# Kernel tuning notes

Measured on AMD Instinct MI355X. Metric: run time of the kernel, lower is better.

## Reference

```python
import jax, jax.numpy as jnp
import numpy as np

T, B, D_IN, H, ALPHA = 512, 32, 41, 800, 20
BOND_LENS = np.array([1.458, 1.525, 1.330], dtype=np.float32)   # N-CA, CA-C, C-N (Angstrom)
BOND_ANGS = np.array([2.124, 1.941, 2.028], dtype=np.float32)   # supplementary bond angles (rad)


def _lstm_dir(x, Wih, Whh, b, reverse):
    # x: [T,B,in] -> hidden states [T,B,H] for one direction
    xs = jnp.einsum('tbi,gi->tbg', x, Wih) + b  # precompute input projections [T,B,4H]
    if reverse:
        xs = xs[::-1]
    h0 = jnp.zeros((x.shape[1], Whh.shape[1]), x.dtype)

    def step(carry, xg):
        h, c = carry
        g = xg + h @ Whh.T
        i, f, gg, o = jnp.split(g, 4, axis=-1)
        c = jax.nn.sigmoid(f) * c + jax.nn.sigmoid(i) * jnp.tanh(gg)
        h = jax.nn.sigmoid(o) * jnp.tanh(c)
        return (h, c), h

    _, hs = jax.lax.scan(step, (h0, h0), xs)
    return hs[::-1] if reverse else hs


def _bilstm(x, Wf, Uf, bf, Wb, Ub, bb):
    return jnp.concatenate([_lstm_dir(x, Wf, Uf, bf, False),
                            _lstm_dir(x, Wb, Ub, bb, True)], axis=-1)


def _calculate_dihedrals(p, alphabet):
    # p: [T,B,ALPHA] softmax weights; alphabet: [ALPHA,3] learned angles
    y = p @ jnp.sin(alphabet)
    xc = p @ jnp.cos(alphabet)
    return jnp.arctan2(y, xc)  # [T,B,3]


def _calculate_coordinates(angles):
    # NeRF-style recursive extension: 3 backbone atoms per residue.
    t, b, _ = angles.shape
    tors = angles.transpose(0, 2, 1).reshape(3 * t, b)          # [3T,B]
    r = jnp.tile(jnp.asarray(BOND_LENS), t)                      # [3T]
    th = jnp.tile(jnp.asarray(BOND_ANGS), t)                     # [3T]
    a0 = jnp.broadcast_to(jnp.array([0.0, 0.0, 0.0], angles.dtype), (b, 3))
    b0 = jnp.broadcast_to(jnp.array([1.458, 0.0, 0.0], angles.dtype), (b, 3))
    c0 = jnp.broadcast_to(jnp.array([2.0, 1.0, 0.0], angles.dtype), (b, 3))

    def _norm(v):
        return v / jnp.linalg.norm(v, axis=-1, keepdims=True)

    def step(carry, inp):
        pa, pb, pc = carry
        phi, rr, tt = inp                                        # phi:[B], rr/tt scalar
        bc = _norm(pc - pb)
        n = _norm(jnp.cross(pb - pa, bc))
        m = jnp.cross(n, bc)
        d = (pc - rr * jnp.cos(tt) * bc
             + (rr * jnp.sin(tt)) * (jnp.cos(phi)[:, None] * m + jnp.sin(phi)[:, None] * n))
        return (pb, pc, d), d

    _, coords = jax.lax.scan(step, (a0, b0, c0), (tors, r, th))
    return coords  # [3T,B,3]


def setup_inputs() -> dict:
    key = jax.random.key(0)
    ks = jax.random.split(key, 16)
    s = 0.05
    d = {"x": jax.random.normal(ks[0], (T, B, D_IN), jnp.float32)}
    ins = [D_IN, 2 * H]
    i = 1
    for l in range(2):
        for dname in ("f", "b"):
            d[f"Wih_{dname}{l}"] = jax.random.normal(ks[i], (4 * H, ins[l]), jnp.float32) * s; i += 1
            d[f"Whh_{dname}{l}"] = jax.random.normal(ks[i], (4 * H, H), jnp.float32) * s; i += 1
            d[f"b_{dname}{l}"] = jnp.zeros((4 * H,), jnp.float32)
    d["Wl"] = jax.random.normal(ks[13], (ALPHA, 2 * H), jnp.float32) * s
    d["bl"] = jnp.zeros((ALPHA,), jnp.float32)
    d["alphabet"] = jax.random.uniform(ks[14], (ALPHA, 3), jnp.float32, -np.pi, np.pi)
    return d


def reference(x, Wih_f0, Whh_f0, b_f0, Wih_b0, Whh_b0, b_b0,
              Wih_f1, Whh_f1, b_f1, Wih_b1, Whh_b1, b_b1,
              Wl, bl, alphabet):
    h1 = _bilstm(x, Wih_f0, Whh_f0, b_f0, Wih_b0, Whh_b0, b_b0)   # [T,B,2H]
    h2 = _bilstm(h1, Wih_f1, Whh_f1, b_f1, Wih_b1, Whh_b1, b_b1)  # [T,B,2H]
    logits = jnp.einsum('tbh,ah->tba', h2, Wl) + bl
    p = jax.nn.softmax(logits, axis=-1)
    angles = _calculate_dihedrals(p, alphabet)                     # [T,B,3]
    return _calculate_coordinates(angles)                          # [3T,B,3]
```

## Files before the change

### kernel.cpp

```cpp
#include <hip/hip_runtime.h>
#include <math.h>


#define TT 512
#define BB 32
#define HH 800
#define DIN 41
#define KROW 1600

typedef _Float16 f16;
typedef _Float16 half8 __attribute__((ext_vector_type(8)));
typedef float floatx4 __attribute__((ext_vector_type(4)));
typedef unsigned uint4v __attribute__((ext_vector_type(4)));

#define OFF_XT   8192
#define OFF_H1   (OFF_XT + 524288)
#define OFF_H2   (OFF_H1 + 13107200)
#define OFF_ANG  (OFF_H2 + 13107200)
#define OFF_SIN  (OFF_ANG + 49152)
#define OFF_COS  (OFF_SIN + 64)

#define SENT 0xFFFFFFFFFFFFFFFFull

__device__ __forceinline__ float sigm(float x) { return 1.0f / (1.0f + expf(-x)); }

union U64H8 { unsigned long long u[2]; half8 h; };

__device__ __forceinline__ unsigned long long ald8(const f16* p) {
    return __hip_atomic_load((const unsigned long long*)p, __ATOMIC_RELAXED, __HIP_MEMORY_SCOPE_AGENT);
}
__device__ __forceinline__ void ast8(f16* p, unsigned long long v) {
    __hip_atomic_store((unsigned long long*)p, v, __ATOMIC_RELAXED, __HIP_MEMORY_SCOPE_AGENT);
}
__device__ __forceinline__ half8 cvt8(const float* p) {
    half8 r;
#pragma unroll
    for (int i = 0; i < 8; ++i) r[i] = (f16)p[i];
    return r;
}

__device__ __forceinline__ size_t hpi(int t, int KT, int q, int b) {
    return ((((size_t)t * 50 + KT) * 4 + q) * 32 + b) * 8;
}

__global__ __launch_bounds__(512, 1) void rnn0_kernel(
    const f16* __restrict__ xp, f16* __restrict__ h1,
    const float* __restrict__ Wih_f0, const float* __restrict__ Whh_f0, const float* __restrict__ b_f0,
    const float* __restrict__ Wih_b0, const float* __restrict__ Whh_b0, const float* __restrict__ b_b0)
{
    __shared__ float gbuf[8][32][34];
    __shared__ f16  hbuf[256];

    const int tid  = threadIdx.x;
    const int w    = tid >> 6;
    const int lane = tid & 63;
    const int l15  = lane & 15;
    const int quad = lane >> 4;
    const int dir  = blockIdx.x / 100;
    const int blk  = blockIdx.x % 100;
    const int j0   = blk * 8;
    const int jl   = tid >> 5;
    const int bb   = tid & 31;

    const float* Wih = dir ? Wih_b0 : Wih_f0;
    const float* Whh = dir ? Whh_b0 : Whh_f0;
    const float* bs  = dir ? b_b0  : b_f0;

    half8 afr[2][4];
#pragma unroll
    for (int mt = 0; mt < 2; ++mt) {
        const int r = mt * 16 + l15;
        const int grow = (r >> 3) * HH + j0 + (r & 7);
#pragma unroll
        for (int i = 0; i < 4; ++i) {
            const int kt = w + 8 * i;
            half8 v;
#pragma unroll
            for (int jj = 0; jj < 8; ++jj) v[jj] = (f16)0.f;
            if (kt < 27) {
                if (kt < 2) {
#pragma unroll
                    for (int jj = 0; jj < 8; ++jj) {
                        const int k = kt * 32 + quad * 8 + jj;
                        if (k < DIN) v[jj] = (f16)Wih[(size_t)grow * DIN + k];
                    }
                } else {
                    v = cvt8(Whh + (size_t)grow * HH + (kt - 2) * 32 + quad * 8);
                }
            }
            afr[mt][i] = v;
        }
    }
    const float bi = bs[0 * HH + j0 + jl], bf = bs[1 * HH + j0 + jl],
                bg = bs[2 * HH + j0 + jl], bo = bs[3 * HH + j0 + jl];

    const int KT0 = dir * 25 + (blk >> 2);
    const int q0  = blk & 3;

    half8 px0, px1;
    {
        const int t0 = dir ? (TT - 1) : 0;
        if (w < 2) {
            const f16* p = xp + ((((size_t)t0 * 2 + w) * 4 + quad) * 32) * 8;
            px0 = *(const half8*)(p + (size_t)l15 * 8);
            px1 = *(const half8*)(p + (size_t)(16 + l15) * 8);
        }
    }

    float creg = 0.0f;
    for (int s = 0; s < TT; ++s) {
        const int t  = dir ? (TT - 1 - s) : s;
        const int tp = dir ? t + 1 : t - 1;
        const int tn = dir ? (t > 0 ? t - 1 : 0) : (t < TT - 1 ? t + 1 : t);

        U64H8 rb[4][2];
        if (s > 0) {
#pragma unroll
            for (int i = 0; i < 4; ++i) {
                const int kt = w + 8 * i;
                if (kt >= 2 && kt < 27) {
                    const f16* p = h1 + hpi(tp, dir * 25 + (kt - 2), quad, 0);
                    rb[i][0].u[0] = ald8(p + (size_t)l15 * 8);
                    rb[i][0].u[1] = ald8(p + (size_t)l15 * 8 + 4);
                    rb[i][1].u[0] = ald8(p + (size_t)(16 + l15) * 8);
                    rb[i][1].u[1] = ald8(p + (size_t)(16 + l15) * 8 + 4);
                }
            }
        }

        floatx4 acc[2][2];
        acc[0][0] = (floatx4)0.f; acc[0][1] = (floatx4)0.f;
        acc[1][0] = (floatx4)0.f; acc[1][1] = (floatx4)0.f;

        if (w < 2) {
            acc[0][0] = __builtin_amdgcn_mfma_f32_16x16x32_f16(afr[0][0], px0, acc[0][0], 0, 0, 0);
            acc[0][1] = __builtin_amdgcn_mfma_f32_16x16x32_f16(afr[0][0], px1, acc[0][1], 0, 0, 0);
            acc[1][0] = __builtin_amdgcn_mfma_f32_16x16x32_f16(afr[1][0], px0, acc[1][0], 0, 0, 0);
            acc[1][1] = __builtin_amdgcn_mfma_f32_16x16x32_f16(afr[1][0], px1, acc[1][1], 0, 0, 0);
            const f16* p = xp + ((((size_t)tn * 2 + w) * 4 + quad) * 32) * 8;
            px0 = *(const half8*)(p + (size_t)l15 * 8);
            px1 = *(const half8*)(p + (size_t)(16 + l15) * 8);
        }

        if (s > 0) {
            int dm = 0;
#pragma unroll
            for (int i = 0; i < 4; ++i) {
                const int kt = w + 8 * i;
                if (kt >= 2 && kt < 27) {
                    const int bad = (rb[i][0].u[0] == SENT) | (rb[i][0].u[1] == SENT) |
                                    (rb[i][1].u[0] == SENT) | (rb[i][1].u[1] == SENT);
                    dm |= bad << i;
                }
            }
            while (__any(dm != 0)) {
#pragma unroll
                for (int i = 0; i < 4; ++i) {
                    const int kt = w + 8 * i;
                    if (kt >= 2 && kt < 27) {
                        if (dm & (1 << i)) {
                            const f16* p = h1 + hpi(tp, dir * 25 + (kt - 2), quad, 0);
                            rb[i][0].u[0] = ald8(p + (size_t)l15 * 8);
                            rb[i][0].u[1] = ald8(p + (size_t)l15 * 8 + 4);
                            rb[i][1].u[0] = ald8(p + (size_t)(16 + l15) * 8);
                            rb[i][1].u[1] = ald8(p + (size_t)(16 + l15) * 8 + 4);
                        }
                    }
                }
                int nm = 0;
#pragma unroll
                for (int i = 0; i < 4; ++i) {
                    const int kt = w + 8 * i;
                    if (kt >= 2 && kt < 27) {
                        if (dm & (1 << i)) {
                            const int bad = (rb[i][0].u[0] == SENT) | (rb[i][0].u[1] == SENT) |
                                            (rb[i][1].u[0] == SENT) | (rb[i][1].u[1] == SENT);
                            nm |= bad << i;
                        }
                    }
                }
                dm = nm;
            }
#pragma unroll
            for (int i = 0; i < 4; ++i) {
                const int kt = w + 8 * i;
                if (kt >= 2 && kt < 27) {
                    acc[0][0] = __builtin_amdgcn_mfma_f32_16x16x32_f16(afr[0][i], rb[i][0].h, acc[0][0], 0, 0, 0);
                    acc[0][1] = __builtin_amdgcn_mfma_f32_16x16x32_f16(afr[0][i], rb[i][1].h, acc[0][1], 0, 0, 0);
                    acc[1][0] = __builtin_amdgcn_mfma_f32_16x16x32_f16(afr[1][i], rb[i][0].h, acc[1][0], 0, 0, 0);
                    acc[1][1] = __builtin_amdgcn_mfma_f32_16x16x32_f16(afr[1][i], rb[i][1].h, acc[1][1], 0, 0, 0);
                }
            }
        }

#pragma unroll
        for (int mt = 0; mt < 2; ++mt)
#pragma unroll
            for (int nt = 0; nt < 2; ++nt)
#pragma unroll
                for (int rg = 0; rg < 4; ++rg)
                    gbuf[w][mt * 16 + quad * 4 + rg][nt * 16 + l15] = acc[mt][nt][rg];
        __syncthreads();
        if (tid < 256) {
            float gi_ = bi, gf_ = bf, gc_ = bg, go_ = bo;
#pragma unroll
            for (int ww = 0; ww < 8; ++ww) {
                gi_ += gbuf[ww][jl][bb];
                gf_ += gbuf[ww][8 + jl][bb];
                gc_ += gbuf[ww][16 + jl][bb];
                go_ += gbuf[ww][24 + jl][bb];
            }
            const float cn = sigm(gf_) * creg + sigm(gi_) * tanhf(gc_);
            creg = cn;
            hbuf[bb * 8 + jl] = (f16)(sigm(go_) * tanhf(cn));
        }
        __syncthreads();
        if (tid < BB) {
            f16* dst = h1 + hpi(t, KT0, q0, tid);
            const unsigned long long* src = (const unsigned long long*)(hbuf + tid * 8);
            ast8(dst, src[0]);
            ast8(dst + 4, src[1]);
        }
    }
}

__global__ __launch_bounds__(512, 1) void rnn1_kernel(
    const f16* __restrict__ h1, f16* __restrict__ h2,
    const float* __restrict__ Wih_f1, const float* __restrict__ Whh_f1, const float* __restrict__ b_f1,
    const float* __restrict__ Wih_b1, const float* __restrict__ Whh_b1, const float* __restrict__ b_b1)
{
    __shared__ float gbuf[8][32][34];
    __shared__ f16  hbuf[256];

    const int tid  = threadIdx.x;
    const int w    = tid >> 6;
    const int lane = tid & 63;
    const int l15  = lane & 15;
    const int quad = lane >> 4;
    const int dir  = blockIdx.x / 100;
    const int blk  = blockIdx.x % 100;
    const int j0   = blk * 8;
    const int jl   = tid >> 5;
    const int bb   = tid & 31;

    const float* Wih = dir ? Wih_b1 : Wih_f1;
    const float* Whh = dir ? Whh_b1 : Whh_f1;
    const float* bs  = dir ? b_b1  : b_f1;

    half8 afr[2][10];
#pragma unroll
    for (int mt = 0; mt < 2; ++mt) {
        const int r = mt * 16 + l15;
        const int grow = (r >> 3) * HH + j0 + (r & 7);
#pragma unroll
        for (int i = 0; i < 10; ++i) {
            const int kt = w + 8 * i;
            half8 v;
#pragma unroll
            for (int jj = 0; jj < 8; ++jj) v[jj] = (f16)0.f;
            if (kt < 75) {
                if (kt < 50) v = cvt8(Wih + (size_t)grow * KROW + kt * 32 + quad * 8);
                else         v = cvt8(Whh + (size_t)grow * HH + (kt - 50) * 32 + quad * 8);
            }
            afr[mt][i] = v;
        }
    }
    const float bi = bs[0 * HH + j0 + jl], bf = bs[1 * HH + j0 + jl],
                bg = bs[2 * HH + j0 + jl], bo = bs[3 * HH + j0 + jl];

    const int KT0 = dir * 25 + (blk >> 2);
    const int q0  = blk & 3;

    half8 pa[7][2];
    {
        const int t0 = dir ? (TT - 1) : 0;
#pragma unroll
        for (int i = 0; i < 7; ++i) {
            const int kt = w + 8 * i;
            if (kt < 50) {
                const f16* p = h1 + hpi(t0, kt, quad, 0);
                pa[i][0] = *(const half8*)(p + (size_t)l15 * 8);
                pa[i][1] = *(const half8*)(p + (size_t)(16 + l15) * 8);
            }
        }
    }

    float creg = 0.0f;
    for (int s = 0; s < TT; ++s) {
        const int t  = dir ? (TT - 1 - s) : s;
        const int tp = dir ? t + 1 : t - 1;
        const int tn = dir ? (t > 0 ? t - 1 : 0) : (t < TT - 1 ? t + 1 : t);

        U64H8 rb[4][2];
        if (s > 0) {
#pragma unroll
            for (int i = 6; i < 10; ++i) {
                const int kt = w + 8 * i;
                if (kt >= 50 && kt < 75) {
                    const f16* p = h2 + hpi(tp, dir * 25 + (kt - 50), quad, 0);
                    rb[i - 6][0].u[0] = ald8(p + (size_t)l15 * 8);
                    rb[i - 6][0].u[1] = ald8(p + (size_t)l15 * 8 + 4);
                    rb[i - 6][1].u[0] = ald8(p + (size_t)(16 + l15) * 8);
                    rb[i - 6][1].u[1] = ald8(p + (size_t)(16 + l15) * 8 + 4);
                }
            }
        }

        floatx4 acc[2][2];
        acc[0][0] = (floatx4)0.f; acc[0][1] = (floatx4)0.f;
        acc[1][0] = (floatx4)0.f; acc[1][1] = (floatx4)0.f;

#pragma unroll
        for (int i = 0; i < 7; ++i) {
            const int kt = w + 8 * i;
            if (kt < 50) {
                acc[0][0] = __builtin_amdgcn_mfma_f32_16x16x32_f16(afr[0][i], pa[i][0], acc[0][0], 0, 0, 0);
                acc[0][1] = __builtin_amdgcn_mfma_f32_16x16x32_f16(afr[0][i], pa[i][1], acc[0][1], 0, 0, 0);
                acc[1][0] = __builtin_amdgcn_mfma_f32_16x16x32_f16(afr[1][i], pa[i][0], acc[1][0], 0, 0, 0);
                acc[1][1] = __builtin_amdgcn_mfma_f32_16x16x32_f16(afr[1][i], pa[i][1], acc[1][1], 0, 0, 0);
            }
        }

#pragma unroll
        for (int i = 0; i < 7; ++i) {
            const int kt = w + 8 * i;
            if (kt < 50) {
                const f16* p = h1 + hpi(tn, kt, quad, 0);
                pa[i][0] = *(const half8*)(p + (size_t)l15 * 8);
                pa[i][1] = *(const half8*)(p + (size_t)(16 + l15) * 8);
            }
        }

        if (s > 0) {
            int dm = 0;
#pragma unroll
            for (int i = 6; i < 10; ++i) {
                const int kt = w + 8 * i;
                if (kt >= 50 && kt < 75) {
                    const int bad = (rb[i - 6][0].u[0] == SENT) | (rb[i - 6][0].u[1] == SENT) |
                                    (rb[i - 6][1].u[0] == SENT) | (rb[i - 6][1].u[1] == SENT);
                    dm |= bad << (i - 6);
                }
            }
            while (__any(dm != 0)) {
#pragma unroll
                for (int i = 6; i < 10; ++i) {
                    const int kt = w + 8 * i;
                    if (kt >= 50 && kt < 75) {
                        if (dm & (1 << (i - 6))) {
                            const f16* p = h2 + hpi(tp, dir * 25 + (kt - 50), quad, 0);
                            rb[i - 6][0].u[0] = ald8(p + (size_t)l15 * 8);
                            rb[i - 6][0].u[1] = ald8(p + (size_t)l15 * 8 + 4);
                            rb[i - 6][1].u[0] = ald8(p + (size_t)(16 + l15) * 8);
                            rb[i - 6][1].u[1] = ald8(p + (size_t)(16 + l15) * 8 + 4);
                        }
                    }
                }
                int nm = 0;
#pragma unroll
                for (int i = 6; i < 10; ++i) {
                    const int kt = w + 8 * i;
                    if (kt >= 50 && kt < 75) {
                        if (dm & (1 << (i - 6))) {
                            const int bad = (rb[i - 6][0].u[0] == SENT) | (rb[i - 6][0].u[1] == SENT) |
                                            (rb[i - 6][1].u[0] == SENT) | (rb[i - 6][1].u[1] == SENT);
                            nm |= bad << (i - 6);
                        }
                    }
                }
                dm = nm;
            }
#pragma unroll
            for (int i = 6; i < 10; ++i) {
                const int kt = w + 8 * i;
                if (kt >= 50 && kt < 75) {
                    acc[0][0] = __builtin_amdgcn_mfma_f32_16x16x32_f16(afr[0][i], rb[i - 6][0].h, acc[0][0], 0, 0, 0);
                    acc[0][1] = __builtin_amdgcn_mfma_f32_16x16x32_f16(afr[0][i], rb[i - 6][1].h, acc[0][1], 0, 0, 0);
                    acc[1][0] = __builtin_amdgcn_mfma_f32_16x16x32_f16(afr[1][i], rb[i - 6][0].h, acc[1][0], 0, 0, 0);
                    acc[1][1] = __builtin_amdgcn_mfma_f32_16x16x32_f16(afr[1][i], rb[i - 6][1].h, acc[1][1], 0, 0, 0);
                }
            }
        }

#pragma unroll
        for (int mt = 0; mt < 2; ++mt)
#pragma unroll
            for (int nt = 0; nt < 2; ++nt)
#pragma unroll
                for (int rg = 0; rg < 4; ++rg)
                    gbuf[w][mt * 16 + quad * 4 + rg][nt * 16 + l15] = acc[mt][nt][rg];
        __syncthreads();
        if (tid < 256) {
            float gi_ = bi, gf_ = bf, gc_ = bg, go_ = bo;
#pragma unroll
            for (int ww = 0; ww < 8; ++ww) {
                gi_ += gbuf[ww][jl][bb];
                gf_ += gbuf[ww][8 + jl][bb];
                gc_ += gbuf[ww][16 + jl][bb];
                go_ += gbuf[ww][24 + jl][bb];
            }
            const float cn = sigm(gf_) * creg + sigm(gi_) * tanhf(gc_);
            creg = cn;
            hbuf[bb * 8 + jl] = (f16)(sigm(go_) * tanhf(cn));
        }
        __syncthreads();
        if (tid < BB) {
            f16* dst = h2 + hpi(t, KT0, q0, tid);
            const unsigned long long* src = (const unsigned long long*)(hbuf + tid * 8);
            ast8(dst, src[0]);
            ast8(dst + 4, src[1]);
        }
    }
}

__global__ void prep_kernel(const float* __restrict__ x, const float* __restrict__ alphabet,
                            f16* __restrict__ xp, float* __restrict__ sin_t,
                            float* __restrict__ cos_t, unsigned* __restrict__ hsent) {
    const int gid = blockIdx.x * blockDim.x + threadIdx.x;
    const int nth = gridDim.x * blockDim.x;
    for (int idx = gid; idx < TT * BB * 64; idx += nth) {
        const int tb = idx >> 6;
        const int i  = idx & 63;
        const int t  = tb >> 5;
        const int b  = tb & 31;
        const size_t di = ((((size_t)t * 2 + (i >> 5)) * 4 + ((i >> 3) & 3)) * 32 + b) * 8 + (i & 7);
        xp[di] = (i < DIN) ? (f16)x[(size_t)tb * DIN + i] : (f16)0.f;
    }
    uint4v* hs4 = (uint4v*)hsent;
    const uint4v sv = {0xFFFFFFFFu, 0xFFFFFFFFu, 0xFFFFFFFFu, 0xFFFFFFFFu};
    const int n4 = (2 * 13107200) / 4;
    for (int idx = gid; idx < n4; idx += nth) hs4[idx] = sv;
    if (gid < 60) { sin_t[gid] = sinf(alphabet[gid]); cos_t[gid] = cosf(alphabet[gid]); }
}

__global__ __launch_bounds__(640, 1) void head_kernel(
    const f16* __restrict__ h2, const float* __restrict__ Wl, const float* __restrict__ bl,
    const float* __restrict__ sin_t, const float* __restrict__ cos_t,
    float* __restrict__ angles) {
    __shared__ float pl[20][33];
    __shared__ float mx[32];
    const int t = blockIdx.x;
    const int a = threadIdx.x / 32;
    const int b = threadIdx.x & 31;
    if (a < 20) {
        float acc = bl[a];
        const float* wr = Wl + (size_t)a * KROW;
        const f16*   hr = h2 + (size_t)t * 50 * 4 * 32 * 8;
        for (int k8 = 0; k8 < KROW / 8; ++k8) {
            const half8 hv = *(const half8*)(hr + (((size_t)k8) * 32 + b) * 8);
#pragma unroll
            for (int j = 0; j < 8; ++j) acc = fmaf(wr[k8 * 8 + j], (float)hv[j], acc);
        }
        pl[a][b] = acc;
    }
    __syncthreads();
    if (threadIdx.x < 32) {
        float m = pl[0][threadIdx.x];
        for (int i = 1; i < 20; ++i) m = fmaxf(m, pl[i][threadIdx.x]);
        mx[threadIdx.x] = m;
    }
    __syncthreads();
    if (a < 20) pl[a][b] = expf(pl[a][b] - mx[b]);
    __syncthreads();
    if (threadIdx.x < 96) {
        const int c = threadIdx.x / 32, b2 = threadIdx.x & 31;
        float y = 0.f, xx = 0.f;
        for (int i = 0; i < 20; ++i) {
            const float e = pl[i][b2];
            y  = fmaf(e, sin_t[i * 3 + c], y);
            xx = fmaf(e, cos_t[i * 3 + c], xx);
        }
        angles[((size_t)t * BB + b2) * 3 + c] = atan2f(y, xx);
    }
}

__global__ void coords_kernel(const float* __restrict__ angles, float* __restrict__ out) {
    const int b = threadIdx.x;
    if (b >= BB) return;
    const float rs[3]  = {1.458f, 1.525f, 1.33f};
    const float ths[3] = {2.124f, 1.941f, 2.028f};
    float ct[3], st[3];
#pragma unroll
    for (int k = 0; k < 3; ++k) { ct[k] = cosf(ths[k]); st[k] = sinf(ths[k]); }
    float pax = 0.f,     pay = 0.f, paz = 0.f;
    float pbx = 1.458f,  pby = 0.f, pbz = 0.f;
    float pcx = 2.f,     pcy = 1.f, pcz = 0.f;
    for (int n = 0; n < 3 * TT; ++n) {
        const int t = n / 3;
        const int k = n - 3 * t;
        const float phi = angles[((size_t)t * BB + b) * 3 + k];
        float ux = pcx - pbx, uy = pcy - pby, uz = pcz - pbz;
        const float il = rsqrtf(ux * ux + uy * uy + uz * uz);
        const float bcx = ux * il, bcy = uy * il, bcz = uz * il;
        const float wx = pbx - pax, wy = pby - pay, wz = pbz - paz;
        float cx = wy * bcz - wz * bcy, cy = wz * bcx - wx * bcz, cz = wx * bcy - wy * bcx;
        const float iln = rsqrtf(cx * cx + cy * cy + cz * cz);
        const float nx = cx * iln, ny = cy * iln, nz = cz * iln;
        const float mxv = ny * bcz - nz * bcy, myv = nz * bcx - nx * bcz, mzv = nx * bcy - ny * bcx;
        float sp, cp;
        __sincosf(phi, &sp, &cp);
        const float rr = rs[k], cth = ct[k], sth = st[k];
        const float dx = pcx - rr * cth * bcx + rr * sth * (cp * mxv + sp * nx);
        const float dy = pcy - rr * cth * bcy + rr * sth * (cp * myv + sp * ny);
        const float dz = pcz - rr * cth * bcz + rr * sth * (cp * mzv + sp * nz);
        float* o = out + ((size_t)n * BB + b) * 3;
        o[0] = dx; o[1] = dy; o[2] = dz;
        pax = pbx; pay = pby; paz = pbz;
        pbx = pcx; pby = pcy; pbz = pcz;
        pcx = dx;  pcy = dy;  pcz = dz;
    }
}

extern "C" void kernel_launch(void* const* d_in, const int* in_sizes, int n_in,
                              void* d_out, int out_size, void* d_ws, size_t ws_size,
                              hipStream_t stream) {
    (void)in_sizes; (void)n_in; (void)out_size; (void)ws_size;
    const float* x      = (const float*)d_in[0];
    const float* Wih_f0 = (const float*)d_in[1];
    const float* Whh_f0 = (const float*)d_in[2];
    const float* b_f0   = (const float*)d_in[3];
    const float* Wih_b0 = (const float*)d_in[4];
    const float* Whh_b0 = (const float*)d_in[5];
    const float* b_b0   = (const float*)d_in[6];
    const float* Wih_f1 = (const float*)d_in[7];
    const float* Whh_f1 = (const float*)d_in[8];
    const float* b_f1   = (const float*)d_in[9];
    const float* Wih_b1 = (const float*)d_in[10];
    const float* Whh_b1 = (const float*)d_in[11];
    const float* b_b1   = (const float*)d_in[12];
    const float* Wl     = (const float*)d_in[13];
    const float* bl     = (const float*)d_in[14];
    const float* alphabet = (const float*)d_in[15];

    float* ws = (float*)d_ws;
    f16*   xp     = (f16*)(ws + OFF_XT);
    f16*   h1     = (f16*)(ws + OFF_H1);
    f16*   h2     = (f16*)(ws + OFF_H2);
    float* angles = ws + OFF_ANG;
    float* sin_t  = ws + OFF_SIN;
    float* cos_t  = ws + OFF_COS;

    prep_kernel<<<1024, 256, 0, stream>>>(x, alphabet, xp, sin_t, cos_t, (unsigned*)(ws + OFF_H1));
    rnn0_kernel<<<200, 512, 0, stream>>>(xp, h1,
        Wih_f0, Whh_f0, b_f0, Wih_b0, Whh_b0, b_b0);
    rnn1_kernel<<<200, 512, 0, stream>>>(h1, h2,
        Wih_f1, Whh_f1, b_f1, Wih_b1, Whh_b1, b_b1);
    head_kernel<<<TT, 640, 0, stream>>>(h2, Wl, bl, sin_t, cos_t, angles);
    coords_kernel<<<1, 64, 0, stream>>>(angles, (float*)d_out);
}
```

Measured before the change: 4.455 ms.

## Halve LSTM persistent blocks by assigning 16 hidden units per block

New measurement: 7.600 ms. 70.6% more time.

```diff
diff --git a/kernel.cpp b/kernel.cpp
--- a/kernel.cpp
+++ b/kernel.cpp
@@ -48,17 +48,17 @@
     const float* __restrict__ Wih_f0, const float* __restrict__ Whh_f0, const float* __restrict__ b_f0,
     const float* __restrict__ Wih_b0, const float* __restrict__ Whh_b0, const float* __restrict__ b_b0)
 {
-    __shared__ float gbuf[8][32][34];
-    __shared__ f16  hbuf[256];
+    __shared__ float gbuf[8][64][34];
+    __shared__ f16  hbuf[512];
 
     const int tid  = threadIdx.x;
     const int w    = tid >> 6;
     const int lane = tid & 63;
     const int l15  = lane & 15;
     const int quad = lane >> 4;
-    const int dir  = blockIdx.x / 100;
-    const int blk  = blockIdx.x % 100;
-    const int j0   = blk * 8;
+    const int dir  = blockIdx.x / 50;
+    const int blk  = blockIdx.x % 50;
+    const int j0   = blk * 16;
     const int jl   = tid >> 5;
     const int bb   = tid & 31;
 
@@ -66,11 +66,10 @@
     const float* Whh = dir ? Whh_b0 : Whh_f0;
     const float* bs  = dir ? b_b0  : b_f0;
 
-    half8 afr[2][4];
-#pragma unroll
-    for (int mt = 0; mt < 2; ++mt) {
-        const int r = mt * 16 + l15;
-        const int grow = (r >> 3) * HH + j0 + (r & 7);
+    half8 afr[4][4];
+#pragma unroll
+    for (int mt = 0; mt < 4; ++mt) {
+        const int grow = mt * HH + j0 + l15;
 #pragma unroll
         for (int i = 0; i < 4; ++i) {
             const int kt = w + 8 * i;
@@ -94,8 +93,9 @@
     const float bi = bs[0 * HH + j0 + jl], bf = bs[1 * HH + j0 + jl],
                 bg = bs[2 * HH + j0 + jl], bo = bs[3 * HH + j0 + jl];
 
-    const int KT0 = dir * 25 + (blk >> 2);
-    const int q0  = blk & 3;
+    const int g8   = blk * 2 + (tid >> 5);
+    const int sKT  = dir * 25 + (g8 >> 2);
+    const int sq   = g8 & 3;
 
     half8 px0, px1;
     {
@@ -128,15 +128,16 @@
             }
         }
 
-        floatx4 acc[2][2];
-        acc[0][0] = (floatx4)0.f; acc[0][1] = (floatx4)0.f;
-        acc[1][0] = (floatx4)0.f; acc[1][1] = (floatx4)0.f;
+        floatx4 acc[4][2];
+#pragma unroll
+        for (int mt = 0; mt < 4; ++mt) { acc[mt][0] = (floatx4)0.f; acc[mt][1] = (floatx4)0.f; }
 
         if (w < 2) {
-            acc[0][0] = __builtin_amdgcn_mfma_f32_16x16x32_f16(afr[0][0], px0, acc[0][0], 0, 0, 0);
-            acc[0][1] = __builtin_amdgcn_mfma_f32_16x16x32_f16(afr[0][0], px1, acc[0][1], 0, 0, 0);
-            acc[1][0] = __builtin_amdgcn_mfma_f32_16x16x32_f16(afr[1][0], px0, acc[1][0], 0, 0, 0);
-            acc[1][1] = __builtin_amdgcn_mfma_f32_16x16x32_f16(afr[1][0], px1, acc[1][1], 0, 0, 0);
+#pragma unroll
+            for (int mt = 0; mt < 4; ++mt) {
+                acc[mt][0] = __builtin_amdgcn_mfma_f32_16x16x32_f16(afr[mt][0], px0, acc[mt][0], 0, 0, 0);
+                acc[mt][1] = __builtin_amdgcn_mfma_f32_16x16x32_f16(afr[mt][0], px1, acc[mt][1], 0, 0, 0);
+            }
             const f16* p = xp + ((((size_t)tn * 2 + w) * 4 + quad) * 32) * 8;
             px0 = *(const half8*)(p + (size_t)l15 * 8);
             px1 = *(const half8*)(p + (size_t)(16 + l15) * 8);
@@ -185,39 +186,41 @@
             for (int i = 0; i < 4; ++i) {
                 const int kt = w + 8 * i;
                 if (kt >= 2 && kt < 27) {
-                    acc[0][0] = __builtin_amdgcn_mfma_f32_16x16x32_f16(afr[0][i], rb[i][0].h, acc[0][0], 0, 0, 0);
-                    acc[0][1] = __builtin_amdgcn_mfma_f32_16x16x32_f16(afr[0][i], rb[i][1].h, acc[0][1], 0, 0, 0);
-                    acc[1][0] = __builtin_amdgcn_mfma_f32_16x16x32_f16(afr[1][i], rb[i][0].h, acc[1][0], 0, 0, 0);
-                    acc[1][1] = __builtin_amdgcn_mfma_f32_16x16x32_f16(afr[1][i], rb[i][1].h, acc[1][1], 0, 0, 0);
-                }
-            }
-        }
-
-#pragma unroll
-        for (int mt = 0; mt < 2; ++mt)
+#pragma unroll
+                    for (int mt = 0; mt < 4; ++mt) {
+                        acc[mt][0] = __builtin_amdgcn_mfma_f32_16x16x32_f16(afr[mt][i], rb[i][0].h, acc[mt][0], 0, 0, 0);
+                        acc[mt][1] = __builtin_amdgcn_mfma_f32_16x16x32_f16(afr[mt][i], rb[i][1].h, acc[mt][1], 0, 0, 0);
+                    }
+                }
+            }
+        }
+
+#pragma unroll
+        for (int mt = 0; mt < 4; ++mt)
 #pragma unroll
             for (int nt = 0; nt < 2; ++nt)
 #pragma unroll
                 for (int rg = 0; rg < 4; ++rg)
                     gbuf[w][mt * 16 + quad * 4 + rg][nt * 16 + l15] = acc[mt][nt][rg];
         __syncthreads();
-        if (tid < 256) {
+        {
             float gi_ = bi, gf_ = bf, gc_ = bg, go_ = bo;
 #pragma unroll
             for (int ww = 0; ww < 8; ++ww) {
                 gi_ += gbuf[ww][jl][bb];
-                gf_ += gbuf[ww][8 + jl][bb];
-                gc_ += gbuf[ww][16 + jl][bb];
-                go_ += gbuf[ww][24 + jl][bb];
+                gf_ += gbuf[ww][16 + jl][bb];
+                gc_ += gbuf[ww][32 + jl][bb];
+                go_ += gbuf[ww][48 + jl][bb];
             }
             const float cn = sigm(gf_) * creg + sigm(gi_) * tanhf(gc_);
             creg = cn;
-            hbuf[bb * 8 + jl] = (f16)(sigm(go_) * tanhf(cn));
+            hbuf[bb * 16 + jl] = (f16)(sigm(go_) * tanhf(cn));
         }
         __syncthreads();
-        if (tid < BB) {
-            f16* dst = h1 + hpi(t, KT0, q0, tid);
-            const unsigned long long* src = (const unsigned long long*)(hbuf + tid * 8);
+        if (tid < 64) {
+            const int b = tid & 31;
+            f16* dst = h1 + hpi(t, sKT, sq, b);
+            const unsigned long long* src = (const unsigned long long*)(hbuf + b * 16 + (tid >> 5) * 8);
             ast8(dst, src[0]);
             ast8(dst + 4, src[1]);
         }
@@ -229,17 +232,17 @@
     const float* __restrict__ Wih_f1, const float* __restrict__ Whh_f1, const float* __restrict__ b_f1,
     const float* __restrict__ Wih_b1, const float* __restrict__ Whh_b1, const float* __restrict__ b_b1)
 {
-    __shared__ float gbuf[8][32][34];
-    __shared__ f16  hbuf[256];
+    __shared__ float gbuf[8][64][34];
+    __shared__ f16  hbuf[512];
 
     const int tid  = threadIdx.x;
     const int w    = tid >> 6;
     const int lane = tid & 63;
     const int l15  = lane & 15;
     const int quad = lane >> 4;
-    const int dir  = blockIdx.x / 100;
-    const int blk  = blockIdx.x % 100;
-    const int j0   = blk * 8;
+    const int dir  = blockIdx.x / 50;
+    const int blk  = blockIdx.x % 50;
+    const int j0   = blk * 16;
     const int jl   = tid >> 5;
     const int bb   = tid & 31;
 
@@ -247,11 +250,10 @@
     const float* Whh = dir ? Whh_b1 : Whh_f1;
     const float* bs  = dir ? b_b1  : b_f1;
 
-    half8 afr[2][10];
-#pragma unroll
-    for (int mt = 0; mt < 2; ++mt) {
-        const int r = mt * 16 + l15;
-        const int grow = (r >> 3) * HH + j0 + (r & 7);
+    half8 afr[4][10];
+#pragma unroll
+    for (int mt = 0; mt < 4; ++mt) {
+        const int grow = mt * HH + j0 + l15;
 #pragma unroll
         for (int i = 0; i < 10; ++i) {
             const int kt = w + 8 * i;
@@ -268,8 +270,9 @@
     const float bi = bs[0 * HH + j0 + jl], bf = bs[1 * HH + j0 + jl],
                 bg = bs[2 * HH + j0 + jl], bo = bs[3 * HH + j0 + jl];
 
-    const int KT0 = dir * 25 + (blk >> 2);
-    const int q0  = blk & 3;
+    const int g8   = blk * 2 + (tid >> 5);
+    const int sKT  = dir * 25 + (g8 >> 2);
+    const int sq   = g8 & 3;
 
     half8 pa[7][2];
     {
@@ -306,18 +309,19 @@
             }
         }
 
-        floatx4 acc[2][2];
-        acc[0][0] = (floatx4)0.f; acc[0][1] = (floatx4)0.f;
-        acc[1][0] = (floatx4)0.f; acc[1][1] = (floatx4)0.f;
+        floatx4 acc[4][2];
+#pragma unroll
+        for (int mt = 0; mt < 4; ++mt) { acc[mt][0] = (floatx4)0.f; acc[mt][1] = (floatx4)0.f; }
 
 #pragma unroll
         for (int i = 0; i < 7; ++i) {
             const int kt = w + 8 * i;
             if (kt < 50) {
-                acc[0][0] = __builtin_amdgcn_mfma_f32_16x16x32_f16(afr[0][i], pa[i][0], acc[0][0], 0, 0, 0);
-                acc[0][1] = __builtin_amdgcn_mfma_f32_16x16x32_f16(afr[0][i], pa[i][1], acc[0][1], 0, 0, 0);
-                acc[1][0] = __builtin_amdgcn_mfma_f32_16x16x32_f16(afr[1][i], pa[i][0], acc[1][0], 0, 0, 0);
-                acc[1][1] = __builtin_amdgcn_mfma_f32_16x16x32_f16(afr[1][i], pa[i][1], acc[1][1], 0, 0, 0);
+#pragma unroll
+                for (int mt = 0; mt < 4; ++mt) {
+                    acc[mt][0] = __builtin_amdgcn_mfma_f32_16x16x32_f16(afr[mt][i], pa[i][0], acc[mt][0], 0, 0, 0);
+                    acc[mt][1] = __builtin_amdgcn_mfma_f32_16x16x32_f16(afr[mt][i], pa[i][1], acc[mt][1], 0, 0, 0);
+                }
             }
         }
 
@@ -374,39 +378,41 @@
             for (int i = 6; i < 10; ++i) {
                 const int kt = w + 8 * i;
                 if (kt >= 50 && kt < 75) {
-                    acc[0][0] = __builtin_amdgcn_mfma_f32_16x16x32_f16(afr[0][i], rb[i - 6][0].h, acc[0][0], 0, 0, 0);
-                    acc[0][1] = __builtin_amdgcn_mfma_f32_16x16x32_f16(afr[0][i], rb[i - 6][1].h, acc[0][1], 0, 0, 0);
-                    acc[1][0] = __builtin_amdgcn_mfma_f32_16x16x32_f16(afr[1][i], rb[i - 6][0].h, acc[1][0], 0, 0, 0);
-                    acc[1][1] = __builtin_amdgcn_mfma_f32_16x16x32_f16(afr[1][i], rb[i - 6][1].h, acc[1][1], 0, 0, 0);
-                }
-            }
-        }
-
-#pragma unroll
-        for (int mt = 0; mt < 2; ++mt)
+#pragma unroll
+                    for (int mt = 0; mt < 4; ++mt) {
+                        acc[mt][0] = __builtin_amdgcn_mfma_f32_16x16x32_f16(afr[mt][i], rb[i - 6][0].h, acc[mt][0], 0, 0, 0);
+                        acc[mt][1] = __builtin_amdgcn_mfma_f32_16x16x32_f16(afr[mt][i], rb[i - 6][1].h, acc[mt][1], 0, 0, 0);
+                    }
+                }
+            }
+        }
+
+#pragma unroll
+        for (int mt = 0; mt < 4; ++mt)
 #pragma unroll
             for (int nt = 0; nt < 2; ++nt)
 #pragma unroll
                 for (int rg = 0; rg < 4; ++rg)
                     gbuf[w][mt * 16 + quad * 4 + rg][nt * 16 + l15] = acc[mt][nt][rg];
         __syncthreads();
-        if (tid < 256) {
+        {
             float gi_ = bi, gf_ = bf, gc_ = bg, go_ = bo;
 #pragma unroll
             for (int ww = 0; ww < 8; ++ww) {
                 gi_ += gbuf[ww][jl][bb];
-                gf_ += gbuf[ww][8 + jl][bb];
-                gc_ += gbuf[ww][16 + jl][bb];
-                go_ += gbuf[ww][24 + jl][bb];
+                gf_ += gbuf[ww][16 + jl][bb];
+                gc_ += gbuf[ww][32 + jl][bb];
+                go_ += gbuf[ww][48 + jl][bb];
             }
             const float cn = sigm(gf_) * creg + sigm(gi_) * tanhf(gc_);
             creg = cn;
-            hbuf[bb * 8 + jl] = (f16)(sigm(go_) * tanhf(cn));
+            hbuf[bb * 16 + jl] = (f16)(sigm(go_) * tanhf(cn));
         }
         __syncthreads();
-        if (tid < BB) {
-            f16* dst = h2 + hpi(t, KT0, q0, tid);
-            const unsigned long long* src = (const unsigned long long*)(hbuf + tid * 8);
+        if (tid < 64) {
+            const int b = tid & 31;
+            f16* dst = h2 + hpi(t, sKT, sq, b);
+            const unsigned long long* src = (const unsigned long long*)(hbuf + b * 16 + (tid >> 5) * 8);
             ast8(dst, src[0]);
             ast8(dst + 4, src[1]);
         }
@@ -541,9 +547,9 @@
     float* cos_t  = ws + OFF_COS;
 
     prep_kernel<<<1024, 256, 0, stream>>>(x, alphabet, xp, sin_t, cos_t, (unsigned*)(ws + OFF_H1));
-    rnn0_kernel<<<200, 512, 0, stream>>>(xp, h1,
+    rnn0_kernel<<<100, 512, 0, stream>>>(xp, h1,
         Wih_f0, Whh_f0, b_f0, Wih_b0, Whh_b0, b_b0);
-    rnn1_kernel<<<200, 512, 0, stream>>>(h1, h2,
+    rnn1_kernel<<<100, 512, 0, stream>>>(h1, h2,
         Wih_f1, Whh_f1, b_f1, Wih_b1, Whh_b1, b_b1);
     head_kernel<<<TT, 640, 0, stream>>>(h2, Wl, bl, sin_t, cos_t, angles);
     coords_kernel<<<1, 64, 0, stream>>>(angles, (float*)d_out);
```
